# Kernel optimization log

Measured on AMD Instinct MI355X. Metric: run time of the kernel, lower is better.

Reference implementation:

```python
import jax, jax.numpy as jnp
import numpy as np

V, A, N, C = 3, 4, 50000, 128


def setup_inputs() -> dict:
    key = jax.random.key(0)
    k1, k2, k3 = jax.random.split(key, 3)
    x = jax.random.normal(k1, (V, A, N, C), dtype=jnp.float32)
    # per-view Linear(in=C, out=C): weight [out,in], bias [out]
    W = jax.random.normal(k2, (V, C, C), dtype=jnp.float32) / np.sqrt(C)
    b = jax.random.normal(k3, (V, C), dtype=jnp.float32) * 0.01
    return {"x": x, "W": W, "b": b}


def reference(x, W, b):
    # per-view linear: out[v,a,n,d] = x[v,a,n,c] @ W[v,d,c]^T + b[v,d]
    out = jnp.einsum('vanc,vdc->vand', x, W) + b[:, None, None, :]
    # view summary: mean over nodes -> [V, A, C]
    s = x.mean(axis=2)
    # attention scores: s . out per node -> [V, A, N]
    scores = jnp.einsum('vac,vanc->van', s, out)
    # tanh then softmax across views (dim 0)
    w = jax.nn.softmax(jnp.tanh(scores), axis=0)
    # weighted combine of views -> [A, N, C]
    return jnp.einsum('van,vanc->anc', w, x)
```

## Files before the change

### kernel.cpp

```cpp
#include <hip/hip_runtime.h>
#include <hip/hip_bf16.h>

#define V 3
#define A 4
#define NN 50000
#define C 128
#define C4 32
#define CHUNKS 128

__global__ void k_colsum(const float* __restrict__ x, float* __restrict__ s_sum) {
    const int va    = blockIdx.y;
    const int chunk = blockIdx.x;
    const int rowsPer = (NN + CHUNKS - 1) / CHUNKS;
    const int n0 = chunk * rowsPer;
    const int n1 = (n0 + rowsPer < NN) ? (n0 + rowsPer) : NN;

    const int lane4 = threadIdx.x & 31;
    const int rowIn = threadIdx.x >> 5;

    const float4* xp = (const float4*)(x + (size_t)va * NN * C);
    float4 acc = {0.f, 0.f, 0.f, 0.f};
    for (int n = n0 + rowIn; n < n1; n += 8) {
        float4 v = xp[(size_t)n * C4 + lane4];
        acc.x += v.x; acc.y += v.y; acc.z += v.z; acc.w += v.w;
    }

    __shared__ float4 red[256];
    red[threadIdx.x] = acc;
    __syncthreads();
    if (threadIdx.x < 32) {
        float4 t = red[threadIdx.x];
        #pragma unroll
        for (int r = 1; r < 8; r++) {
            float4 o = red[threadIdx.x + 32 * r];
            t.x += o.x; t.y += o.y; t.z += o.z; t.w += o.w;
        }
        float* dst = s_sum + va * C + lane4 * 4;
        atomicAdd(dst + 0, t.x);
        atomicAdd(dst + 1, t.y);
        atomicAdd(dst + 2, t.z);
        atomicAdd(dst + 3, t.w);
    }
}

__global__ void k_tvec(const float* __restrict__ s_sum, const float* __restrict__ W,
                       const float* __restrict__ b, float* __restrict__ t,
                       float* __restrict__ c0) {
    const int va = blockIdx.x;
    const int v  = va / A;
    const int c  = threadIdx.x;

    __shared__ float sb[C];
    __shared__ float pb[C];
    const float invN = 1.0f / (float)NN;
    sb[c] = s_sum[va * C + c] * invN;
    __syncthreads();

    const float* Wv = W + (size_t)v * C * C;
    float acc = 0.f;
    #pragma unroll 8
    for (int d = 0; d < C; d++) acc += sb[d] * Wv[d * C + c];
    t[va * C + c] = acc;

    pb[c] = sb[c] * b[v * C + c];
    __syncthreads();
    if (c == 0) {
        float s = 0.f;
        for (int d = 0; d < C; d++) s += pb[d];
        c0[va] = s;
    }
}

__global__ void k_main(const float* __restrict__ x, const float* __restrict__ t,
                       const float* __restrict__ c0, float* __restrict__ out) {
    const int lane = threadIdx.x & 31;
    const int grp  = threadIdx.x >> 5;
    const int n    = blockIdx.x * 8 + grp;
    const int a    = blockIdx.y;

    const size_t vstride = (size_t)A * NN * C4;
    const float4* xp = (const float4*)x;
    const size_t base = ((size_t)a * NN + n) * C4 + lane;

    float4 x0 = xp[base];
    float4 x1 = xp[base + vstride];
    float4 x2 = xp[base + 2 * vstride];

    const float4* tp = (const float4*)t;
    float4 t0 = tp[(0 * A + a) * C4 + lane];
    float4 t1 = tp[(1 * A + a) * C4 + lane];
    float4 t2 = tp[(2 * A + a) * C4 + lane];

    float d0 = x0.x * t0.x + x0.y * t0.y + x0.z * t0.z + x0.w * t0.w;
    float d1 = x1.x * t1.x + x1.y * t1.y + x1.z * t1.z + x1.w * t1.w;
    float d2 = x2.x * t2.x + x2.y * t2.y + x2.z * t2.z + x2.w * t2.w;

    #pragma unroll
    for (int off = 16; off > 0; off >>= 1) {
        d0 += __shfl_xor(d0, off, 32);
        d1 += __shfl_xor(d1, off, 32);
        d2 += __shfl_xor(d2, off, 32);
    }

    float s0 = tanhf(d0 + c0[0 * A + a]);
    float s1 = tanhf(d1 + c0[1 * A + a]);
    float s2 = tanhf(d2 + c0[2 * A + a]);

    float m  = fmaxf(s0, fmaxf(s1, s2));
    float e0 = expf(s0 - m), e1 = expf(s1 - m), e2 = expf(s2 - m);
    float inv = 1.0f / (e0 + e1 + e2);
    float w0 = e0 * inv, w1 = e1 * inv, w2 = e2 * inv;

    float4 o;
    o.x = w0 * x0.x + w1 * x1.x + w2 * x2.x;
    o.y = w0 * x0.y + w1 * x1.y + w2 * x2.y;
    o.z = w0 * x0.z + w1 * x1.z + w2 * x2.z;
    o.w = w0 * x0.w + w1 * x1.w + w2 * x2.w;

    ((float4*)out)[((size_t)a * NN + n) * C4 + lane] = o;
}

extern "C" void kernel_launch(void* const* d_in, const int* in_sizes, int n_in,
                              void* d_out, int out_size, void* d_ws, size_t ws_size,
                              hipStream_t stream) {
    const float* x = (const float*)d_in[0];
    const float* W = (const float*)d_in[1];
    const float* b = (const float*)d_in[2];
    float* out = (float*)d_out;

    float* s_sum = (float*)d_ws;
    float* t     = s_sum + V * A * C;
    float* c0    = t + V * A * C;

    hipMemsetAsync(s_sum, 0, V * A * C * sizeof(float), stream);

    k_colsum<<<dim3(CHUNKS, V * A), 256, 0, stream>>>(x, s_sum);
    k_tvec<<<V * A, C, 0, stream>>>(s_sum, W, b, t, c0);
    k_main<<<dim3(NN / 8, A), 256, 0, stream>>>(x, t, c0, out);
}
```

Before: 502.7 us.

## Replace atomics with partial sums, drop memset, two rows per warp, fast math

The column-sum kernel now writes per-chunk partial sums instead of doing atomicAdd, so the memset launch goes away and k_tvec reduces the partials itself. k_tvec also switches its bias dot product from a serial loop to a tree reduction. The main kernel handles two node rows per 32-lane group, halving the grid and adding memory-level parallelism. It replaces tanhf, expf and the division with intrinsic fast versions, which carries a small accuracy risk.

```diff
diff --git a/kernel.cpp b/kernel.cpp
--- a/kernel.cpp
+++ b/kernel.cpp
@@ -7,13 +7,25 @@
 #define C 128
 #define C4 32
 #define CHUNKS 128
+#define ROWS_PER ((NN + CHUNKS - 1) / CHUNKS)
+#define VA (V * A)
 
-__global__ void k_colsum(const float* __restrict__ x, float* __restrict__ s_sum) {
+__device__ __forceinline__ float dot4(float4 a, float4 b) {
+    return a.x * b.x + a.y * b.y + a.z * b.z + a.w * b.w;
+}
+
+__device__ __forceinline__ float fast_tanh(float x) {
+    float ax = fminf(fabsf(x), 15.f);
+    float e  = __expf(2.f * ax);
+    float r  = (e - 1.f) * __frcp_rn(e + 1.f);
+    return copysignf(r, x);
+}
+
+__global__ void k_colsum(const float* __restrict__ x, float* __restrict__ part) {
     const int va    = blockIdx.y;
     const int chunk = blockIdx.x;
-    const int rowsPer = (NN + CHUNKS - 1) / CHUNKS;
-    const int n0 = chunk * rowsPer;
-    const int n1 = (n0 + rowsPer < NN) ? (n0 + rowsPer) : NN;
+    const int n0 = chunk * ROWS_PER;
+    const int n1 = (n0 + ROWS_PER < NN) ? (n0 + ROWS_PER) : NN;
 
     const int lane4 = threadIdx.x & 31;
     const int rowIn = threadIdx.x >> 5;
@@ -35,89 +47,112 @@
             float4 o = red[threadIdx.x + 32 * r];
             t.x += o.x; t.y += o.y; t.z += o.z; t.w += o.w;
         }
-        float* dst = s_sum + va * C + lane4 * 4;
-        atomicAdd(dst + 0, t.x);
-        atomicAdd(dst + 1, t.y);
-        atomicAdd(dst + 2, t.z);
-        atomicAdd(dst + 3, t.w);
+        ((float4*)part)[((size_t)chunk * VA + va) * C4 + lane4] = t;
     }
 }
 
-__global__ void k_tvec(const float* __restrict__ s_sum, const float* __restrict__ W,
+__global__ void k_tvec(const float* __restrict__ part, const float* __restrict__ W,
                        const float* __restrict__ b, float* __restrict__ t,
                        float* __restrict__ c0) {
     const int va = blockIdx.x;
     const int v  = va / A;
     const int c  = threadIdx.x;
 
+    float acc = 0.f;
+    #pragma unroll 4
+    for (int ch = 0; ch < CHUNKS; ch++)
+        acc += part[((size_t)ch * VA + va) * C + c];
+
     __shared__ float sb[C];
     __shared__ float pb[C];
-    const float invN = 1.0f / (float)NN;
-    sb[c] = s_sum[va * C + c] * invN;
+    sb[c] = acc * (1.0f / (float)NN);
     __syncthreads();
 
     const float* Wv = W + (size_t)v * C * C;
-    float acc = 0.f;
+    float t_acc = 0.f;
     #pragma unroll 8
-    for (int d = 0; d < C; d++) acc += sb[d] * Wv[d * C + c];
-    t[va * C + c] = acc;
+    for (int d = 0; d < C; d++) t_acc += sb[d] * Wv[d * C + c];
+    t[va * C + c] = t_acc;
 
     pb[c] = sb[c] * b[v * C + c];
     __syncthreads();
-    if (c == 0) {
-        float s = 0.f;
-        for (int d = 0; d < C; d++) s += pb[d];
-        c0[va] = s;
+    #pragma unroll
+    for (int s = 64; s > 0; s >>= 1) {
+        if (c < s) pb[c] += pb[c + s];
+        __syncthreads();
     }
+    if (c == 0) c0[va] = pb[0];
 }
 
 __global__ void k_main(const float* __restrict__ x, const float* __restrict__ t,
                        const float* __restrict__ c0, float* __restrict__ out) {
     const int lane = threadIdx.x & 31;
     const int grp  = threadIdx.x >> 5;
-    const int n    = blockIdx.x * 8 + grp;
     const int a    = blockIdx.y;
+    const int n0   = blockIdx.x * 16 + grp * 2;
 
     const size_t vstride = (size_t)A * NN * C4;
     const float4* xp = (const float4*)x;
-    const size_t base = ((size_t)a * NN + n) * C4 + lane;
+    const size_t baseA = ((size_t)a * NN + n0) * C4 + lane;
+    const size_t baseB = baseA + C4;
 
-    float4 x0 = xp[base];
-    float4 x1 = xp[base + vstride];
-    float4 x2 = xp[base + 2 * vstride];
+    float4 xa0 = xp[baseA];
+    float4 xa1 = xp[baseA + vstride];
+    float4 xa2 = xp[baseA + 2 * vstride];
+    float4 xb0 = xp[baseB];
+    float4 xb1 = xp[baseB + vstride];
+    float4 xb2 = xp[baseB + 2 * vstride];
 
     const float4* tp = (const float4*)t;
     float4 t0 = tp[(0 * A + a) * C4 + lane];
     float4 t1 = tp[(1 * A + a) * C4 + lane];
     float4 t2 = tp[(2 * A + a) * C4 + lane];
 
-    float d0 = x0.x * t0.x + x0.y * t0.y + x0.z * t0.z + x0.w * t0.w;
-    float d1 = x1.x * t1.x + x1.y * t1.y + x1.z * t1.z + x1.w * t1.w;
-    float d2 = x2.x * t2.x + x2.y * t2.y + x2.z * t2.z + x2.w * t2.w;
+    float da0 = dot4(xa0, t0), da1 = dot4(xa1, t1), da2 = dot4(xa2, t2);
+    float db0 = dot4(xb0, t0), db1 = dot4(xb1, t1), db2 = dot4(xb2, t2);
 
     #pragma unroll
     for (int off = 16; off > 0; off >>= 1) {
-        d0 += __shfl_xor(d0, off, 32);
-        d1 += __shfl_xor(d1, off, 32);
-        d2 += __shfl_xor(d2, off, 32);
+        da0 += __shfl_xor(da0, off, 32);
+        da1 += __shfl_xor(da1, off, 32);
+        da2 += __shfl_xor(da2, off, 32);
+        db0 += __shfl_xor(db0, off, 32);
+        db1 += __shfl_xor(db1, off, 32);
+        db2 += __shfl_xor(db2, off, 32);
     }
 
-    float s0 = tanhf(d0 + c0[0 * A + a]);
-    float s1 = tanhf(d1 + c0[1 * A + a]);
-    float s2 = tanhf(d2 + c0[2 * A + a]);
+    const float cc0 = c0[0 * A + a], cc1 = c0[1 * A + a], cc2 = c0[2 * A + a];
 
-    float m  = fmaxf(s0, fmaxf(s1, s2));
-    float e0 = expf(s0 - m), e1 = expf(s1 - m), e2 = expf(s2 - m);
-    float inv = 1.0f / (e0 + e1 + e2);
-    float w0 = e0 * inv, w1 = e1 * inv, w2 = e2 * inv;
+    float sa0 = fast_tanh(da0 + cc0);
+    float sa1 = fast_tanh(da1 + cc1);
+    float sa2 = fast_tanh(da2 + cc2);
+    float ma  = fmaxf(sa0, fmaxf(sa1, sa2));
+    float ea0 = __expf(sa0 - ma), ea1 = __expf(sa1 - ma), ea2 = __expf(sa2 - ma);
+    float inva = __frcp_rn(ea0 + ea1 + ea2);
+    float wa0 = ea0 * inva, wa1 = ea1 * inva, wa2 = ea2 * inva;
 
-    float4 o;
-    o.x = w0 * x0.x + w1 * x1.x + w2 * x2.x;
-    o.y = w0 * x0.y + w1 * x1.y + w2 * x2.y;
-    o.z = w0 * x0.z + w1 * x1.z + w2 * x2.z;
-    o.w = w0 * x0.w + w1 * x1.w + w2 * x2.w;
+    float sb0 = fast_tanh(db0 + cc0);
+    float sb1 = fast_tanh(db1 + cc1);
+    float sb2 = fast_tanh(db2 + cc2);
+    float mb  = fmaxf(sb0, fmaxf(sb1, sb2));
+    float eb0 = __expf(sb0 - mb), eb1 = __expf(sb1 - mb), eb2 = __expf(sb2 - mb);
+    float invb = __frcp_rn(eb0 + eb1 + eb2);
+    float wb0 = eb0 * invb, wb1 = eb1 * invb, wb2 = eb2 * invb;
 
-    ((float4*)out)[((size_t)a * NN + n) * C4 + lane] = o;
+    float4 oa, ob;
+    oa.x = wa0 * xa0.x + wa1 * xa1.x + wa2 * xa2.x;
+    oa.y = wa0 * xa0.y + wa1 * xa1.y + wa2 * xa2.y;
+    oa.z = wa0 * xa0.z + wa1 * xa1.z + wa2 * xa2.z;
+    oa.w = wa0 * xa0.w + wa1 * xa1.w + wa2 * xa2.w;
+    ob.x = wb0 * xb0.x + wb1 * xb1.x + wb2 * xb2.x;
+    ob.y = wb0 * xb0.y + wb1 * xb1.y + wb2 * xb2.y;
+    ob.z = wb0 * xb0.z + wb1 * xb1.z + wb2 * xb2.z;
+    ob.w = wb0 * xb0.w + wb1 * xb1.w + wb2 * xb2.w;
+
+    float4* op = (float4*)out;
+    const size_t obase = ((size_t)a * NN + n0) * C4 + lane;
+    op[obase]      = oa;
+    op[obase + C4] = ob;
 }
 
 extern "C" void kernel_launch(void* const* d_in, const int* in_sizes, int n_in,
@@ -128,13 +163,11 @@
     const float* b = (const float*)d_in[2];
     float* out = (float*)d_out;
 
-    float* s_sum = (float*)d_ws;
-    float* t     = s_sum + V * A * C;
-    float* c0    = t + V * A * C;
+    float* part = (float*)d_ws;
+    float* t    = part + (size_t)CHUNKS * VA * C;
+    float* c0   = t + VA * C;
 
-    hipMemsetAsync(s_sum, 0, V * A * C * sizeof(float), stream);
-
-    k_colsum<<<dim3(CHUNKS, V * A), 256, 0, stream>>>(x, s_sum);
-    k_tvec<<<V * A, C, 0, stream>>>(s_sum, W, b, t, c0);
-    k_main<<<dim3(NN / 8, A), 256, 0, stream>>>(x, t, c0, out);
+    k_colsum<<<dim3(CHUNKS, VA), 256, 0, stream>>>(x, part);
+    k_tvec<<<VA, C, 0, stream>>>(part, W, b, t, c0);
+    k_main<<<dim3(NN / 16, A), 256, 0, stream>>>(x, t, c0, out);
 }
```

Result: no change. 506.0 us (+0.7%).
